# Optimization experiments

Hardware: AMD Instinct MI355X
Metric: run time of the kernel (lower is better)

Reference implementation:

```python
import jax, jax.numpy as jnp
import numpy as np

L, NH, H, V, MAXP = 12, 12, 768, 50257, 1024
HD = H // NH
EPS = 1e-5


def setup_inputs() -> dict:
    key = jax.random.key(0)
    ks = iter(jax.random.split(key, 32))
    s = 0.02
    inp = {
        "input_ids": jax.random.randint(next(ks), (8, 1024), 0, V),
        "tok_emb": jax.random.normal(next(ks), (V, H), jnp.float32) * s,
        "pos_emb": jax.random.normal(next(ks), (MAXP, H), jnp.float32) * s,
        "ln1_g": jnp.ones((L, H), jnp.float32),
        "ln1_b": jnp.zeros((L, H), jnp.float32),
        "w_attn": jax.random.normal(next(ks), (L, H, 3 * H), jnp.float32) * s,
        "b_attn": jnp.zeros((L, 3 * H), jnp.float32),
        "w_out": jax.random.normal(next(ks), (L, H, H), jnp.float32) * s,
        "b_out": jnp.zeros((L, H), jnp.float32),
        "ln2_g": jnp.ones((L, H), jnp.float32),
        "ln2_b": jnp.zeros((L, H), jnp.float32),
        "w1": jax.random.normal(next(ks), (L, H, 4 * H), jnp.float32) * s,
        "b1": jnp.zeros((L, 4 * H), jnp.float32),
        "w2": jax.random.normal(next(ks), (L, 4 * H, H), jnp.float32) * s,
        "b2": jnp.zeros((L, H), jnp.float32),
        "lnf_g": jnp.ones((H,), jnp.float32),
        "lnf_b": jnp.zeros((H,), jnp.float32),
    }
    return inp


def _ln(x, g, b):
    mu = jnp.mean(x, axis=-1, keepdims=True)
    var = jnp.var(x, axis=-1, keepdims=True)
    return (x - mu) * jax.lax.rsqrt(var + EPS) * g + b


def _gpt2_forward(input_ids, tok_emb, pos_emb, ln1_g, ln1_b, w_attn, b_attn,
                  w_out, b_out, ln2_g, ln2_b, w1, b1, w2, b2, lnf_g, lnf_b):
    B, S = input_ids.shape
    x = tok_emb[input_ids] + pos_emb[:S]  # [B,S,H]
    # causal mask: True above the diagonal (future positions)
    mask = jnp.triu(jnp.ones((S, S), dtype=bool), k=1)
    inv_sqrt_hd = 1.0 / np.sqrt(HD)
    for l in range(L):
        n1 = _ln(x, ln1_g[l], ln1_b[l])
        qkv = n1 @ w_attn[l] + b_attn[l]  # [B,S,3H]
        q, k, v = jnp.split(qkv, 3, axis=-1)
        q = q.reshape(B, S, NH, HD).transpose(0, 2, 1, 3)
        k = k.reshape(B, S, NH, HD).transpose(0, 2, 1, 3)
        v = v.reshape(B, S, NH, HD).transpose(0, 2, 1, 3)
        scores = jnp.einsum('bhtd,bhsd->bhts', q, k)  # [B,NH,S,S]
        # faithful to source: mask with -10000 BEFORE dividing by sqrt(head_size)
        scores = jnp.where(mask, -10000.0, scores) * inv_sqrt_hd
        probs = jax.nn.softmax(scores, axis=-1)
        attn = jnp.einsum('bhts,bhsd->bhtd', probs, v)
        attn = attn.transpose(0, 2, 1, 3).reshape(B, S, H)
        attn = attn @ w_out[l] + b_out[l]
        x = x + attn
        n2 = _ln(x, ln2_g[l], ln2_b[l])
        h = jax.nn.gelu(n2 @ w1[l] + b1[l], approximate=False)
        x = x + (h @ w2[l] + b2[l])
    x = _ln(x, lnf_g, lnf_b)
    final_encoding = x[:, -1]  # [B,H]
    logits = final_encoding @ tok_emb.T  # tied weights, [B,V]
    return logits, final_encoding


def reference(input_ids, tok_emb, pos_emb, ln1_g, ln1_b, w_attn, b_attn,
              w_out, b_out, ln2_g, ln2_b, w1, b1, w2, b2, lnf_g, lnf_b):
    return _gpt2_forward(input_ids, tok_emb, pos_emb, ln1_g, ln1_b, w_attn,
                         b_attn, w_out, b_out, ln2_g, ln2_b, w1, b1, w2, b2,
                         lnf_g, lnf_b)
```

## Files before the change

### kernel.cpp

```cpp
#include <hip/hip_runtime.h>
#include <cmath>

typedef unsigned short u16;
typedef __bf16 bf16;
typedef __attribute__((ext_vector_type(8))) bf16 bf16x8;
typedef __attribute__((ext_vector_type(4))) float f32x4;

#define DINL __device__ __forceinline__

#define BB 8
#define SS 1024
#define HH 768
#define LL 12
#define NHH 12
#define HDD 64
#define MM 8192
#define VV 50257

DINL u16 f2bf(float f) {
    unsigned int u = __builtin_bit_cast(unsigned int, f);
    u += 0x7fff + ((u >> 16) & 1);
    return (u16)(u >> 16);
}

DINL bf16x8 ld_bf8(const u16* p) { return *(const bf16x8*)p; }

typedef __attribute__((address_space(1))) unsigned int as1_u32;
typedef __attribute__((address_space(3))) unsigned int as3_u32;

DINL void gllds16(const void* g, void* l) {
    __builtin_amdgcn_global_load_lds((as1_u32*)g, (as3_u32*)l, 16, 0, 0);
}

#define BARRIER()                                   \
    do {                                            \
        asm volatile("" ::: "memory");              \
        __builtin_amdgcn_s_barrier();               \
        asm volatile("" ::: "memory");              \
    } while (0)

DINL void xcd_remap(int gx, int& mTile, int& nTile) {
    int i = blockIdx.y * gx + blockIdx.x;
    int xcd = i & 7, j = i >> 3;
    nTile = j % gx;
    mTile = (j / gx) * 8 + xcd;
}

__global__ __launch_bounds__(256) void k_embed(const int* __restrict__ ids,
                                               const float* __restrict__ tok,
                                               const float* __restrict__ pos,
                                               float* __restrict__ x) {
    int tk = blockIdx.x;
    int s = tk & (SS - 1);
    int id = ids[tk];
    const float* tr = tok + (size_t)id * HH;
    const float* pr = pos + (size_t)s * HH;
    float* xr = x + (size_t)tk * HH;
#pragma unroll
    for (int j = 0; j < 3; j++) {
        int d = threadIdx.x + j * 256;
        xr[d] = tr[d] + pr[d];
    }
}

__global__ __launch_bounds__(256) void k_tcvt(const float* __restrict__ src, u16* __restrict__ dst,
                                              int R, int C, size_t sstr, size_t dstr) {
    src += (size_t)blockIdx.z * sstr;
    dst += (size_t)blockIdx.z * dstr;
    __shared__ float t[32][33];
    int tx = threadIdx.x & 31, ty = threadIdx.x >> 5;
    int c0 = blockIdx.x * 32, r0 = blockIdx.y * 32;
#pragma unroll
    for (int p = 0; p < 4; p++)
        t[ty + p * 8][tx] = src[(size_t)(r0 + ty + p * 8) * C + c0 + tx];
    __syncthreads();
#pragma unroll
    for (int p = 0; p < 4; p++)
        dst[(size_t)(c0 + ty + p * 8) * R + r0 + tx] = f2bf(t[tx][ty + p * 8]);
}

template <bool F32OUT>
__global__ __launch_bounds__(256) void k_ln(const float* __restrict__ x, const float* __restrict__ g,
                                            const float* __restrict__ b, void* __restrict__ outp,
                                            int nrows, int rs, int ro) {
    int w = threadIdx.x >> 6, lane = threadIdx.x & 63;
    int row = blockIdx.x * 4 + w;
    if (row >= nrows) return;
    const float4* xr = (const float4*)(x + ((size_t)row * rs + ro) * HH);
    float4 v[3];
    float s = 0.f, s2 = 0.f;
#pragma unroll
    for (int j = 0; j < 3; j++) {
        v[j] = xr[lane + 64 * j];
        s += v[j].x + v[j].y + v[j].z + v[j].w;
        s2 += v[j].x * v[j].x + v[j].y * v[j].y + v[j].z * v[j].z + v[j].w * v[j].w;
    }
#pragma unroll
    for (int off = 32; off; off >>= 1) {
        s += __shfl_xor(s, off, 64);
        s2 += __shfl_xor(s2, off, 64);
    }
    float mu = s * (1.0f / HH);
    float rstd = rsqrtf(s2 * (1.0f / HH) - mu * mu + 1e-5f);
#pragma unroll
    for (int j = 0; j < 3; j++) {
        int d4 = lane + 64 * j;
        float4 gv = ((const float4*)g)[d4];
        float4 bv = ((const float4*)b)[d4];
        float o0 = (v[j].x - mu) * rstd * gv.x + bv.x;
        float o1 = (v[j].y - mu) * rstd * gv.y + bv.y;
        float o2 = (v[j].z - mu) * rstd * gv.z + bv.z;
        float o3 = (v[j].w - mu) * rstd * gv.w + bv.w;
        if (F32OUT) {
            ((float4*)outp)[(size_t)row * (HH / 4) + d4] = make_float4(o0, o1, o2, o3);
        } else {
            ushort4 pk;
            pk.x = f2bf(o0); pk.y = f2bf(o1); pk.z = f2bf(o2); pk.w = f2bf(o3);
            *(ushort4*)((u16*)outp + (size_t)row * HH + d4 * 4) = pk;
        }
    }
}

template <int EPI>
__global__ __launch_bounds__(256) void k_gemm(const u16* __restrict__ A, const u16* __restrict__ BT,
                                              const float* __restrict__ bias,
                                              u16* __restrict__ obuf, u16* __restrict__ qb,
                                              u16* __restrict__ kb, u16* __restrict__ vb,
                                              int N, int K) {
    __shared__ u16 As[3][128 * 32];
    __shared__ u16 Bs[3][128 * 32];
    const int t = threadIdx.x, w = t >> 6, lane = t & 63;
    const int l15 = lane & 15, l4 = lane >> 4;
    const int wr = w >> 1, wc = w & 1;
    int mT, nT;
    xcd_remap(gridDim.x, mT, nT);
    const int m0 = mT * 128, n0 = nT * 128;
    const int KT = K >> 5;

    f32x4 acc[4][4] = {};

    auto stage = [&](int buf, int kt) {
#pragma unroll
        for (int i = 0; i < 2; i++) {
            int idx = w * 2 + i;
            int row = idx * 16 + (lane >> 2);
            int kc = kt * 32 + (((lane & 3) ^ ((lane >> 3) & 3)) * 8);
            gllds16(A + (size_t)(m0 + row) * K + kc, &As[buf][idx * 512]);
            gllds16(BT + (size_t)(n0 + row) * K + kc, &Bs[buf][idx * 512]);
        }
    };

    stage(0, 0);
    stage(1, 1);
    const int sw = (l15 >> 1) & 3;

    for (int kt = 0; kt < KT; ++kt) {
        if (kt + 1 < KT) asm volatile("s_waitcnt vmcnt(4)" ::: "memory");
        else             asm volatile("s_waitcnt vmcnt(0)" ::: "memory");
        BARRIER();

        const u16* ap = As[kt % 3];
        const u16* bp = Bs[kt % 3];
        bf16x8 af[4], bfr[4];
#pragma unroll
        for (int i = 0; i < 4; i++) af[i] = ld_bf8(ap + (wr * 64 + i * 16 + l15) * 32 + ((l4 ^ sw) * 8));
#pragma unroll
        for (int j = 0; j < 4; j++) bfr[j] = ld_bf8(bp + (wc * 64 + j * 16 + l15) * 32 + ((l4 ^ sw) * 8));

        if (kt + 2 < KT) stage((kt + 2) % 3, kt + 2);

        __builtin_amdgcn_s_setprio(1);
#pragma unroll
        for (int i = 0; i < 4; i++)
#pragma unroll
            for (int j = 0; j < 4; j++)
                acc[i][j] = __builtin_amdgcn_mfma_f32_16x16x32_bf16(af[i], bfr[j], acc[i][j], 0, 0, 0);
        __builtin_amdgcn_s_setprio(0);
    }

#pragma unroll
    for (int i = 0; i < 4; i++) {
#pragma unroll
        for (int j = 0; j < 4; j++) {
#pragma unroll
            for (int r = 0; r < 4; r++) {
                int row = m0 + wr * 64 + i * 16 + l4 * 4 + r;
                int n = n0 + wc * 64 + j * 16 + l15;
                float v = acc[i][j][r] + bias[n];
                if (EPI == 0) {
                    int sg = n / HH, wi = n % HH;
                    int h = wi >> 6, d = wi & 63;
                    int bi = row >> 10, s = row & (SS - 1);
                    size_t bh = (size_t)(bi * NHH + h);
                    if (sg == 0)
                        qb[(bh * SS + s) * HDD + d] = f2bf(v * 0.1803368801111204f);
                    else if (sg == 1)
                        kb[(bh * SS + s) * HDD + d] = f2bf(v);
                    else
                        vb[(bh * HDD + d) * SS + s] = f2bf(v);
                } else {
                    float gl = 0.5f * v * (1.0f + erff(v * 0.70710678118654752f));
                    obuf[(size_t)row * N + n] = f2bf(gl);
                }
            }
        }
    }
}

__global__ __launch_bounds__(256) void k_gemm64(const u16* __restrict__ A, const u16* __restrict__ BT,
                                                const float* __restrict__ bias, float* __restrict__ xio,
                                                int N, int K) {
    __shared__ u16 As[3][128 * 32];
    __shared__ u16 Bs[3][64 * 32];
    const int t = threadIdx.x, w = t >> 6, lane = t & 63;
    const int l15 = lane & 15, l4 = lane >> 4;
    const int wr = w >> 1, wc = w & 1;
    int mT, nT;
    xcd_remap(gridDim.x, mT, nT);
    const int m0 = mT * 128, n0 = nT * 64;
    const int KT = K >> 5;

    f32x4 acc[4][2] = {};

    auto stage = [&](int buf, int kt) {
        int rr = lane >> 2;
        int kc = kt * 32 + (((lane & 3) ^ ((lane >> 3) & 3)) * 8);
#pragma unroll
        for (int i = 0; i < 2; i++) {
            int idx = w * 2 + i;
            gllds16(A + (size_t)(m0 + idx * 16 + rr) * K + kc, &As[buf][idx * 512]);
        }
        gllds16(BT + (size_t)(n0 + w * 16 + rr) * K + kc, &Bs[buf][w * 512]);
    };

    stage(0, 0);
    stage(1, 1);
    const int sw = (l15 >> 1) & 3;

    for (int kt = 0; kt < KT; ++kt) {
        if (kt + 1 < KT) asm volatile("s_waitcnt vmcnt(3)" ::: "memory");
        else             asm volatile("s_waitcnt vmcnt(0)" ::: "memory");
        BARRIER();

        const u16* ap = As[kt % 3];
        const u16* bp = Bs[kt % 3];
        bf16x8 af[4], bfr[2];
#pragma unroll
        for (int i = 0; i < 4; i++) af[i] = ld_bf8(ap + (wr * 64 + i * 16 + l15) * 32 + ((l4 ^ sw) * 8));
#pragma unroll
        for (int j = 0; j < 2; j++) bfr[j] = ld_bf8(bp + (wc * 32 + j * 16 + l15) * 32 + ((l4 ^ sw) * 8));

        if (kt + 2 < KT) stage((kt + 2) % 3, kt + 2);

        __builtin_amdgcn_s_setprio(1);
#pragma unroll
        for (int i = 0; i < 4; i++)
#pragma unroll
            for (int j = 0; j < 2; j++)
                acc[i][j] = __builtin_amdgcn_mfma_f32_16x16x32_bf16(af[i], bfr[j], acc[i][j], 0, 0, 0);
        __builtin_amdgcn_s_setprio(0);
    }

#pragma unroll
    for (int i = 0; i < 4; i++) {
#pragma unroll
        for (int j = 0; j < 2; j++) {
#pragma unroll
            for (int r = 0; r < 4; r++) {
                int row = m0 + wr * 64 + i * 16 + l4 * 4 + r;
                int n = n0 + wc * 32 + j * 16 + l15;
                xio[(size_t)row * N + n] += acc[i][j][r] + bias[n];
            }
        }
    }
}

__global__ __launch_bounds__(256) void k_attn(const u16* __restrict__ q, const u16* __restrict__ k,
                                              const u16* __restrict__ vt, u16* __restrict__ o) {
    int qt = 15 - blockIdx.x;
    int bh = blockIdx.y;
    int w = threadIdx.x >> 6, lane = threadIdx.x & 63;
    int l15 = lane & 15, l4 = lane >> 4;

    __shared__ u16 Ks[2][64 * 64];
    __shared__ u16 Vs[2][64 * 64];
    __shared__ u16 pl[4][16 * 72];
    u16* pw = pl[w];

    const size_t bhq = (size_t)bh * SS * HDD;
    int qrow0 = qt * 64 + w * 16;

    auto stage = [&](int buf, int kvb) {
#pragma unroll
        for (int i = 0; i < 2; i++) {
            int rl = w * 16 + i * 8 + (lane >> 3);
            int c = lane & 7;
            int sc = (c ^ (rl & 7)) * 8;
            gllds16(k + bhq + (size_t)(kvb * 64 + rl) * HDD + sc, &Ks[buf][(w * 16 + i * 8) * 64]);
            gllds16(vt + ((size_t)bh * HDD + rl) * SS + kvb * 64 + sc, &Vs[buf][(w * 16 + i * 8) * 64]);
        }
    };

    bf16x8 aq[2];
#pragma unroll
    for (int ks = 0; ks < 2; ks++)
        aq[ks] = ld_bf8(q + bhq + (size_t)(qrow0 + l15) * HDD + ks * 32 + l4 * 8);

    f32x4 acc[4] = {};
    float mrun[4], psum[4];
#pragma unroll
    for (int r = 0; r < 4; r++) { mrun[r] = -1e30f; psum[r] = 0.f; }

    stage(0, 0);
    __syncthreads();
    int buf = 0;

    for (int kvb = 0; kvb <= qt; ++kvb) {
        if (kvb < qt) stage(buf ^ 1, kvb + 1);

        f32x4 s[4] = {};
#pragma unroll
        for (int c = 0; c < 4; c++) {
#pragma unroll
            for (int ks = 0; ks < 2; ks++) {
                bf16x8 kf = ld_bf8(&Ks[buf][(c * 16 + l15) * 64 + ((ks * 4 + l4) ^ (l15 & 7)) * 8]);
                s[c] = __builtin_amdgcn_mfma_f32_16x16x32_bf16(aq[ks], kf, s[c], 0, 0, 0);
            }
        }
        if (kvb == qt) {
#pragma unroll
            for (int c = 0; c < 4; c++) {
                int kvi = kvb * 64 + c * 16 + l15;
#pragma unroll
                for (int r = 0; r < 4; r++) {
                    int qi = qrow0 + l4 * 4 + r;
                    if (kvi > qi) s[c][r] = -1803.3688f;
                }
            }
        }
        float lmax[4];
        int ok = 1;
#pragma unroll
        for (int r = 0; r < 4; r++) {
            lmax[r] = fmaxf(fmaxf(s[0][r], s[1][r]), fmaxf(s[2][r], s[3][r]));
            ok &= (lmax[r] <= mrun[r] + 11.5416f) ? 1 : 0;
        }
        if (!__all(ok)) {
#pragma unroll
            for (int off = 1; off < 16; off <<= 1)
#pragma unroll
                for (int r = 0; r < 4; r++) lmax[r] = fmaxf(lmax[r], __shfl_xor(lmax[r], off, 64));
#pragma unroll
            for (int r = 0; r < 4; r++) {
                float mnew = fmaxf(mrun[r], lmax[r]);
                float ef = __builtin_amdgcn_exp2f(mrun[r] - mnew);
                mrun[r] = mnew;
                psum[r] *= ef;
#pragma unroll
                for (int cd = 0; cd < 4; cd++) acc[cd][r] *= ef;
            }
        }
#pragma unroll
        for (int c = 0; c < 4; c++)
#pragma unroll
            for (int r = 0; r < 4; r++) {
                float pv = __builtin_amdgcn_exp2f(s[c][r] - mrun[r]);
                psum[r] += pv;
                pw[(l4 * 4 + r) * 72 + c * 16 + l15] = f2bf(pv);
            }
#pragma unroll
        for (int ks = 0; ks < 2; ks++) {
            bf16x8 pa = ld_bf8(pw + l15 * 72 + ks * 32 + l4 * 8);
#pragma unroll
            for (int cd = 0; cd < 4; cd++) {
                bf16x8 vf = ld_bf8(&Vs[buf][(cd * 16 + l15) * 64 + ((ks * 4 + l4) ^ (l15 & 7)) * 8]);
                acc[cd] = __builtin_amdgcn_mfma_f32_16x16x32_bf16(pa, vf, acc[cd], 0, 0, 0);
            }
        }
        __syncthreads();
        buf ^= 1;
    }

#pragma unroll
    for (int off = 1; off < 16; off <<= 1)
#pragma unroll
        for (int r = 0; r < 4; r++) psum[r] += __shfl_xor(psum[r], off, 64);

    int b = bh / NHH, h = bh % NHH;
#pragma unroll
    for (int cd = 0; cd < 4; cd++) {
#pragma unroll
        for (int r = 0; r < 4; r++) {
            int qi = qrow0 + l4 * 4 + r;
            float ov = acc[cd][r] / psum[r];
            o[((size_t)b * SS + qi) * HH + h * HDD + cd * 16 + l15] = f2bf(ov);
        }
    }
}

__global__ __launch_bounds__(256) void k_logits(const float* __restrict__ enc,
                                                const float* __restrict__ tok,
                                                float* __restrict__ out) {
    int w = threadIdx.x >> 6, lane = threadIdx.x & 63;
    int v = blockIdx.x * 4 + w;
    if (v >= VV) return;
    const float4* tr = (const float4*)(tok + (size_t)v * HH);
    float a[8];
#pragma unroll
    for (int b = 0; b < 8; b++) a[b] = 0.f;
#pragma unroll
    for (int j = 0; j < 3; j++) {
        float4 t4 = tr[lane + 64 * j];
#pragma unroll
        for (int b = 0; b < 8; b++) {
            float4 e4 = *(const float4*)(enc + (size_t)b * HH + (lane + 64 * j) * 4);
            a[b] += t4.x * e4.x + t4.y * e4.y + t4.z * e4.z + t4.w * e4.w;
        }
    }
#pragma unroll
    for (int off = 32; off; off >>= 1)
#pragma unroll
        for (int b = 0; b < 8; b++) a[b] += __shfl_xor(a[b], off, 64);
    if (lane == 0) {
#pragma unroll
        for (int b = 0; b < 8; b++) out[(size_t)b * VV + v] = a[b];
    }
}

extern "C" void kernel_launch(void* const* d_in, const int* in_sizes, int n_in,
                              void* d_out, int out_size, void* d_ws, size_t ws_size,
                              hipStream_t stream) {
    const int* ids = (const int*)d_in[0];
    const float* tok = (const float*)d_in[1];
    const float* pos = (const float*)d_in[2];
    const float* ln1g = (const float*)d_in[3];
    const float* ln1b = (const float*)d_in[4];
    const float* wat = (const float*)d_in[5];
    const float* bat = (const float*)d_in[6];
    const float* wou = (const float*)d_in[7];
    const float* bou = (const float*)d_in[8];
    const float* ln2g = (const float*)d_in[9];
    const float* ln2b = (const float*)d_in[10];
    const float* w1 = (const float*)d_in[11];
    const float* b1 = (const float*)d_in[12];
    const float* w2 = (const float*)d_in[13];
    const float* b2 = (const float*)d_in[14];
    const float* lnfg = (const float*)d_in[15];
    const float* lnfb = (const float*)d_in[16];

    char* ws = (char*)d_ws;
    float* xw = (float*)(ws + 0);
    u16* nb = (u16*)(ws + 25165824);
    u16* qb = (u16*)(ws + 37748736);
    u16* kb = (u16*)(ws + 50331648);
    u16* vb = (u16*)(ws + 62914560);
    u16* ab = (u16*)(ws + 75497472);
    u16* hb = (u16*)(ws + 88080384);
    u16* wt = (u16*)(ws + 138412032);
    const size_t LSTR = 7077888;
    const size_t WAO = 0, WOO = 1769472, W1O = 2359296, W2O = 4718592;

    float* outf = (float*)d_out;
    float* enc = outf + (size_t)BB * VV;

    k_embed<<<MM, 256, 0, stream>>>(ids, tok, pos, xw);
    k_tcvt<<<dim3(72, 24, 12), 256, 0, stream>>>(wat, wt + WAO, 768, 2304, (size_t)768 * 2304, LSTR);
    k_tcvt<<<dim3(24, 24, 12), 256, 0, stream>>>(wou, wt + WOO, 768, 768, (size_t)768 * 768, LSTR);
    k_tcvt<<<dim3(96, 24, 12), 256, 0, stream>>>(w1, wt + W1O, 768, 3072, (size_t)768 * 3072, LSTR);
    k_tcvt<<<dim3(24, 96, 12), 256, 0, stream>>>(w2, wt + W2O, 3072, 768, (size_t)3072 * 768, LSTR);

    for (int l = 0; l < LL; l++) {
        const u16* wl = wt + (size_t)l * LSTR;
        k_ln<false><<<MM / 4, 256, 0, stream>>>(xw, ln1g + l * HH, ln1b + l * HH, nb, MM, 1, 0);
        k_gemm<0><<<dim3(18, 64), 256, 0, stream>>>(nb, wl + WAO, bat + (size_t)l * 2304,
                                                    nullptr, qb, kb, vb, 2304, 768);
        k_attn<<<dim3(16, 96), 256, 0, stream>>>(qb, kb, vb, ab);
        k_gemm64<<<dim3(12, 64), 256, 0, stream>>>(ab, wl + WOO, bou + (size_t)l * HH, xw, 768, 768);
        k_ln<false><<<MM / 4, 256, 0, stream>>>(xw, ln2g + l * HH, ln2b + l * HH, nb, MM, 1, 0);
        k_gemm<2><<<dim3(24, 64), 256, 0, stream>>>(nb, wl + W1O, b1 + (size_t)l * 3072,
                                                    hb, nullptr, nullptr, nullptr, 3072, 768);
        k_gemm64<<<dim3(12, 64), 256, 0, stream>>>(hb, wl + W2O, b2 + (size_t)l * HH, xw, 768, 3072);
    }
    k_ln<true><<<2, 256, 0, stream>>>(xw, lnfg, lnfb, enc, BB, SS, SS - 1);
    k_logits<<<(VV + 3) / 4, 256, 0, stream>>>(enc, tok, outf);
}
```

Baseline: 3.848 ms.

## Pipeline attention K/V loads with triple-buffered K and explicit vmcnt waits

```diff
diff --git a/kernel.cpp b/kernel.cpp
--- a/kernel.cpp
+++ b/kernel.cpp
@@ -282,7 +282,7 @@
     int w = threadIdx.x >> 6, lane = threadIdx.x & 63;
     int l15 = lane & 15, l4 = lane >> 4;
 
-    __shared__ u16 Ks[2][64 * 64];
+    __shared__ u16 Ks[3][64 * 64];
     __shared__ u16 Vs[2][64 * 64];
     __shared__ u16 pl[4][16 * 72];
     u16* pw = pl[w];
@@ -290,14 +290,20 @@
     const size_t bhq = (size_t)bh * SS * HDD;
     int qrow0 = qt * 64 + w * 16;
 
-    auto stage = [&](int buf, int kvb) {
+    auto stageK = [&](int slot, int kvb) {
 #pragma unroll
         for (int i = 0; i < 2; i++) {
             int rl = w * 16 + i * 8 + (lane >> 3);
-            int c = lane & 7;
-            int sc = (c ^ (rl & 7)) * 8;
-            gllds16(k + bhq + (size_t)(kvb * 64 + rl) * HDD + sc, &Ks[buf][(w * 16 + i * 8) * 64]);
-            gllds16(vt + ((size_t)bh * HDD + rl) * SS + kvb * 64 + sc, &Vs[buf][(w * 16 + i * 8) * 64]);
+            int sc = ((lane & 7) ^ (rl & 7)) * 8;
+            gllds16(k + bhq + (size_t)(kvb * 64 + rl) * HDD + sc, &Ks[slot][(w * 16 + i * 8) * 64]);
+        }
+    };
+    auto stageV = [&](int slot, int kvb) {
+#pragma unroll
+        for (int i = 0; i < 2; i++) {
+            int rl = w * 16 + i * 8 + (lane >> 3);
+            int sc = ((lane & 7) ^ (rl & 7)) * 8;
+            gllds16(vt + ((size_t)bh * HDD + rl) * SS + kvb * 64 + sc, &Vs[slot][(w * 16 + i * 8) * 64]);
         }
     };
 
@@ -311,19 +317,26 @@
 #pragma unroll
     for (int r = 0; r < 4; r++) { mrun[r] = -1e30f; psum[r] = 0.f; }
 
-    stage(0, 0);
-    __syncthreads();
-    int buf = 0;
+    stageK(0, 0);
+    stageV(0, 0);
+    if (qt >= 1) stageK(1, 1);
 
     for (int kvb = 0; kvb <= qt; ++kvb) {
-        if (kvb < qt) stage(buf ^ 1, kvb + 1);
+        if (kvb < qt) asm volatile("s_waitcnt vmcnt(2)" ::: "memory");
+        else          asm volatile("s_waitcnt vmcnt(0)" ::: "memory");
+        BARRIER();
+        if (kvb + 1 <= qt) stageV((kvb + 1) & 1, kvb + 1);
+        if (kvb + 2 <= qt) stageK((kvb + 2) % 3, kvb + 2);
+
+        const u16* kp = Ks[kvb % 3];
+        const u16* vp = Vs[kvb & 1];
 
         f32x4 s[4] = {};
 #pragma unroll
         for (int c = 0; c < 4; c++) {
 #pragma unroll
             for (int ks = 0; ks < 2; ks++) {
-                bf16x8 kf = ld_bf8(&Ks[buf][(c * 16 + l15) * 64 + ((ks * 4 + l4) ^ (l15 & 7)) * 8]);
+                bf16x8 kf = ld_bf8(kp + (c * 16 + l15) * 64 + ((ks * 4 + l4) ^ (l15 & 7)) * 8);
                 s[c] = __builtin_amdgcn_mfma_f32_16x16x32_bf16(aq[ks], kf, s[c], 0, 0, 0);
             }
         }
@@ -373,12 +386,10 @@
             bf16x8 pa = ld_bf8(pw + l15 * 72 + ks * 32 + l4 * 8);
 #pragma unroll
             for (int cd = 0; cd < 4; cd++) {
-                bf16x8 vf = ld_bf8(&Vs[buf][(cd * 16 + l15) * 64 + ((ks * 4 + l4) ^ (l15 & 7)) * 8]);
+                bf16x8 vf = ld_bf8(vp + (cd * 16 + l15) * 64 + ((ks * 4 + l4) ^ (l15 & 7)) * 8);
                 acc[cd] = __builtin_amdgcn_mfma_f32_16x16x32_bf16(pa, vf, acc[cd], 0, 0, 0);
             }
         }
-        __syncthreads();
-        buf ^= 1;
     }
 
 #pragma unroll
```

After: 3.859 ms. No clear change (+0.3%).
